# Kernel tuning notes

Hardware: AMD Instinct MI355X
Metric: run time of the kernel (lower is better)

Reference implementation:

```python
import jax, jax.numpy as jnp
import numpy as np

N = 50000      # nodes
E = 800000     # edges (avg degree 16)
D = 64         # input_dim
L = 64         # latent_dim


def setup_inputs() -> dict:
    key = jax.random.key(0)
    k1, k2, k3, k4, k5, k6 = jax.random.split(key, 6)
    x = jax.random.normal(k1, (N, D), dtype=jnp.float32)
    weight = jax.random.normal(k2, (D, L), dtype=jnp.float32) / np.sqrt(D)
    bias = jax.random.normal(k3, (L,), dtype=jnp.float32) * 0.01
    # strictly positive degrees to keep division well-behaved
    node_degree = jax.random.uniform(k4, (N, 1), dtype=jnp.float32) + 1.0
    edge_src = jax.random.randint(k5, (E,), 0, N, dtype=jnp.int32)
    edge_dst = jax.random.randint(k6, (E,), 0, N, dtype=jnp.int32)
    return {"x": x, "weight": weight, "bias": bias,
            "node_degree": node_degree,
            "edge_src": edge_src, "edge_dst": edge_dst}


def reference(x, weight, bias, node_degree, edge_src, edge_dst):
    # gnn_spmm(adj, x): sparse aggregate over incoming edges -> [N, D]
    agg = jax.ops.segment_sum(x[edge_src], edge_dst, num_segments=N)
    pooled = agg + x                      # residual self-connection
    node_linear = pooled @ weight + bias  # dense projection [N, L]
    normalized = node_linear / node_degree  # normalize_embedding == 2
    return jax.nn.relu(normalized)
```

## Files before the change

kernel.cpp:

```cpp
#include <hip/hip_runtime.h>
#include <hip/hip_fp16.h>

#define N_NODES 50000
#define DIM 64
#define CB 391
#define CAP 2560
#define EB 6400
#define PLW 68
#define SCAP 1344

typedef _Float16 half8 __attribute__((ext_vector_type(8)));
typedef _Float16 half4v __attribute__((ext_vector_type(4)));
typedef float floatx4 __attribute__((ext_vector_type(4)));

#define WS_CURSOR  0
#define WS_COARSE  2048
#define WS_XH      (WS_COARSE + 4003840)
#define WS_WT      (WS_XH + 6400000)

__global__ void __launch_bounds__(256) prep_kernel(
        const float* __restrict__ x, const float* __restrict__ W,
        const int* __restrict__ edge_src, const int* __restrict__ edge_dst,
        _Float16* __restrict__ xh, _Float16* __restrict__ wt,
        int* __restrict__ bucket_cursor, unsigned int* __restrict__ coarse,
        int E, int pa) {
    int b = blockIdx.x, t = threadIdx.x;
    if (b < pa) {
        __shared__ int lhist[CB];
        __shared__ int lbase[CB];
        for (int i = t; i < CB; i += 256) lhist[i] = 0;
        __syncthreads();

        int base = b * EB;
        int end = base + EB; if (end > E) end = E;

        for (int i = base + t; i < end; i += 256) {
            atomicAdd(&lhist[edge_dst[i] >> 7], 1);
        }
        __syncthreads();
        for (int i = t; i < CB; i += 256) {
            lbase[i] = atomicAdd(&bucket_cursor[i], lhist[i]);
            lhist[i] = 0;
        }
        __syncthreads();
        for (int i = base + t; i < end; i += 256) {
            int s = edge_src[i];
            int d = edge_dst[i];
            int bk = d >> 7;
            int r = atomicAdd(&lhist[bk], 1);
            coarse[(size_t)bk * CAP + lbase[bk] + r] =
                ((unsigned int)s << 7) | (unsigned int)(d & 127);
        }
    } else if (b < pa + 3125) {
        int i = (b - pa) * 256 + t;
        float4 v = reinterpret_cast<const float4*>(x)[i];
        half4v h = { (_Float16)v.x, (_Float16)v.y, (_Float16)v.z, (_Float16)v.w };
        reinterpret_cast<half4v*>(xh)[i] = h;
    } else {
        #pragma unroll
        for (int i = 0; i < 16; ++i) {
            int idx = t * 16 + i;
            int n = idx >> 6, k = idx & 63;
            wt[idx] = (_Float16)W[k * DIM + n];
        }
    }
}

__global__ void __launch_bounds__(256) fused_kernel(
        const float* __restrict__ x,
        const _Float16* __restrict__ xh,
        const _Float16* __restrict__ wt,
        const float* __restrict__ bias,
        const float* __restrict__ deg,
        const int* __restrict__ bucket_cursor,
        const unsigned int* __restrict__ coarse,
        float* __restrict__ out) {
    __shared__ unsigned int sedges[SCAP];
    __shared__ float pl[64 * PLW];
    __shared__ int hist[64];
    __shared__ int excl[64];
    __shared__ int cur[64];

    int t = threadIdx.x;
    int b = blockIdx.x;
    int bucket = b >> 1;
    int half = b & 1;
    int nb = b * 64;
    int cnt = bucket_cursor[bucket];
    const unsigned int* cbk = coarse + (size_t)bucket * CAP;

    if (t < 64) hist[t] = 0;
    __syncthreads();
    for (int i = t; i < cnt; i += 256) {
        unsigned int e = cbk[i];
        int loc = (int)(e & 127u);
        if ((loc >> 6) == half) atomicAdd(&hist[loc & 63], 1);
    }
    __syncthreads();

    if (t < 64) {
        int v = hist[t];
        int s = v;
        #pragma unroll
        for (int off = 1; off < 64; off <<= 1) {
            int u = __shfl_up(s, off);
            if (t >= off) s += u;
        }
        excl[t] = s - v;
        cur[t]  = s - v;
    }
    __syncthreads();

    for (int i = t; i < cnt; i += 256) {
        unsigned int e = cbk[i];
        int loc = (int)(e & 127u);
        if ((loc >> 6) == half) {
            int p = atomicAdd(&cur[loc & 63], 1);
            sedges[p] = e >> 7;
        }
    }
    __syncthreads();

    int g = t >> 3;
    int c = t & 7;
    #pragma unroll
    for (int pass = 0; pass < 2; ++pass) {
        int loc = g + pass * 32;
        int node = nb + loc;
        float acc[8];
        #pragma unroll
        for (int j = 0; j < 8; ++j) acc[j] = 0.f;
        int off = excl[loc];
        int ct = (node < N_NODES) ? hist[loc] : 0;
        int k = 0;
        for (; k + 4 <= ct; k += 4) {
            int s0 = (int)sedges[off + k + 0];
            int s1 = (int)sedges[off + k + 1];
            int s2 = (int)sedges[off + k + 2];
            int s3 = (int)sedges[off + k + 3];
            half8 v0 = *reinterpret_cast<const half8*>(xh + (size_t)s0 * DIM + c * 8);
            half8 v1 = *reinterpret_cast<const half8*>(xh + (size_t)s1 * DIM + c * 8);
            half8 v2 = *reinterpret_cast<const half8*>(xh + (size_t)s2 * DIM + c * 8);
            half8 v3 = *reinterpret_cast<const half8*>(xh + (size_t)s3 * DIM + c * 8);
            #pragma unroll
            for (int j = 0; j < 8; ++j) {
                acc[j] += (float)v0[j]; acc[j] += (float)v1[j];
                acc[j] += (float)v2[j]; acc[j] += (float)v3[j];
            }
        }
        for (; k < ct; ++k) {
            int s0 = (int)sedges[off + k];
            half8 v0 = *reinterpret_cast<const half8*>(xh + (size_t)s0 * DIM + c * 8);
            #pragma unroll
            for (int j = 0; j < 8; ++j) acc[j] += (float)v0[j];
        }
        if (node < N_NODES) {
            const float4 r0 = *reinterpret_cast<const float4*>(
                x + (size_t)node * DIM + c * 8);
            const float4 r1 = *reinterpret_cast<const float4*>(
                x + (size_t)node * DIM + c * 8 + 4);
            float* p = &pl[loc * PLW + c * 8];
            p[0] = acc[0] + r0.x; p[1] = acc[1] + r0.y;
            p[2] = acc[2] + r0.z; p[3] = acc[3] + r0.w;
            p[4] = acc[4] + r1.x; p[5] = acc[5] + r1.y;
            p[6] = acc[6] + r1.z; p[7] = acc[7] + r1.w;
        }
    }
    __syncthreads();

    int wv = t >> 6;
    int lane = t & 63;
    int m = lane & 15;
    int q = lane >> 4;
    int lbase = wv * 16;

    const float* ap = &pl[(lbase + m) * PLW];
    half8 a0, a1;
    #pragma unroll
    for (int j = 0; j < 8; ++j) a0[j] = (_Float16)ap[q * 8 + j];
    #pragma unroll
    for (int j = 0; j < 8; ++j) a1[j] = (_Float16)ap[32 + q * 8 + j];

    floatx4 acc4[4];
    #pragma unroll
    for (int tt = 0; tt < 4; ++tt) {
        half8 b0 = *reinterpret_cast<const half8*>(wt + (size_t)(tt * 16 + m) * DIM + q * 8);
        half8 b1 = *reinterpret_cast<const half8*>(wt + (size_t)(tt * 16 + m) * DIM + q * 8 + 32);
        floatx4 cfrag = {0.f, 0.f, 0.f, 0.f};
        cfrag = __builtin_amdgcn_mfma_f32_16x16x32_f16(a0, b0, cfrag, 0, 0, 0);
        cfrag = __builtin_amdgcn_mfma_f32_16x16x32_f16(a1, b1, cfrag, 0, 0, 0);
        acc4[tt] = cfrag;
    }

    #pragma unroll
    for (int r = 0; r < 4; ++r) {
        int row = q * 4 + r;
        int node = nb + lbase + row;
        if (node < N_NODES) {
            float inv = 1.0f / deg[node];
            #pragma unroll
            for (int tt = 0; tt < 4; ++tt) {
                float v = (acc4[tt][r] + bias[tt * 16 + m]) * inv;
                out[(size_t)node * DIM + tt * 16 + m] = fmaxf(v, 0.f);
            }
        }
    }
}

extern "C" void kernel_launch(void* const* d_in, const int* in_sizes, int n_in,
                              void* d_out, int out_size, void* d_ws, size_t ws_size,
                              hipStream_t stream) {
    const float* x        = (const float*)d_in[0];
    const float* weight   = (const float*)d_in[1];
    const float* bias     = (const float*)d_in[2];
    const float* node_deg = (const float*)d_in[3];
    const int*   edge_src = (const int*)d_in[4];
    const int*   edge_dst = (const int*)d_in[5];
    float* out = (float*)d_out;
    const int E = in_sizes[4];

    char* ws = (char*)d_ws;
    int*          bucket_cursor = (int*)(ws + WS_CURSOR);
    unsigned int* coarse        = (unsigned int*)(ws + WS_COARSE);
    _Float16*     xh            = (_Float16*)(ws + WS_XH);
    _Float16*     wt            = (_Float16*)(ws + WS_WT);

    hipMemsetAsync(bucket_cursor, 0, CB * sizeof(int), stream);

    int pa = (E + EB - 1) / EB;
    prep_kernel<<<pa + 3125 + 1, 256, 0, stream>>>(
        x, weight, edge_src, edge_dst, xh, wt, bucket_cursor, coarse, E, pa);

    fused_kernel<<<2 * CB, 256, 0, stream>>>(
        x, xh, wt, bias, node_deg, bucket_cursor, coarse, out);
}
```

Measured before the change: 120.1 us.

## Drop fp16 copy of x, gather fp32 directly, split buckets into sub-cursors

Removes the prep pass that converted x to fp16 and gathers the fp32 rows directly in the aggregation, with 16 threads per node over four passes. The edge bucketing now uses smaller edge blocks (1024) and 8 sub-bucket cursors per coarse bucket, so many more prep blocks run with less contention on each global atomic cursor. The fused kernel walks the 8 sub-bucket segments per bucket. This saves the conversion traffic, but each gathered row is twice as many bytes, and the fixed sub-bucket capacity (384) could overflow under skewed degree distributions.

```diff
diff --git a/kernel.cpp b/kernel.cpp
--- a/kernel.cpp
+++ b/kernel.cpp
@@ -4,26 +4,24 @@
 #define N_NODES 50000
 #define DIM 64
 #define CB 391
-#define CAP 2560
-#define EB 6400
+#define SUBS 8
+#define CAPS 384
+#define EB 1024
+#define SCAP 1344
 #define PLW 68
-#define SCAP 1344
 
 typedef _Float16 half8 __attribute__((ext_vector_type(8)));
-typedef _Float16 half4v __attribute__((ext_vector_type(4)));
 typedef float floatx4 __attribute__((ext_vector_type(4)));
 
 #define WS_CURSOR  0
-#define WS_COARSE  2048
-#define WS_XH      (WS_COARSE + 4003840)
-#define WS_WT      (WS_XH + 6400000)
+#define WS_COARSE  16384
+#define WS_WT      (WS_COARSE + 4804608)
 
 __global__ void __launch_bounds__(256) prep_kernel(
-        const float* __restrict__ x, const float* __restrict__ W,
+        const float* __restrict__ W,
         const int* __restrict__ edge_src, const int* __restrict__ edge_dst,
-        _Float16* __restrict__ xh, _Float16* __restrict__ wt,
-        int* __restrict__ bucket_cursor, unsigned int* __restrict__ coarse,
-        int E, int pa) {
+        int* __restrict__ cursor2, unsigned int* __restrict__ coarse2,
+        _Float16* __restrict__ wt, int E, int pa) {
     int b = blockIdx.x, t = threadIdx.x;
     if (b < pa) {
         __shared__ int lhist[CB];
@@ -31,6 +29,7 @@
         for (int i = t; i < CB; i += 256) lhist[i] = 0;
         __syncthreads();
 
+        int sub = b & (SUBS - 1);
         int base = b * EB;
         int end = base + EB; if (end > E) end = E;
 
@@ -39,7 +38,7 @@
         }
         __syncthreads();
         for (int i = t; i < CB; i += 256) {
-            lbase[i] = atomicAdd(&bucket_cursor[i], lhist[i]);
+            lbase[i] = atomicAdd(&cursor2[sub * CB + i], lhist[i]);
             lhist[i] = 0;
         }
         __syncthreads();
@@ -48,14 +47,9 @@
             int d = edge_dst[i];
             int bk = d >> 7;
             int r = atomicAdd(&lhist[bk], 1);
-            coarse[(size_t)bk * CAP + lbase[bk] + r] =
+            coarse2[((size_t)bk * SUBS + sub) * CAPS + lbase[bk] + r] =
                 ((unsigned int)s << 7) | (unsigned int)(d & 127);
         }
-    } else if (b < pa + 3125) {
-        int i = (b - pa) * 256 + t;
-        float4 v = reinterpret_cast<const float4*>(x)[i];
-        half4v h = { (_Float16)v.x, (_Float16)v.y, (_Float16)v.z, (_Float16)v.w };
-        reinterpret_cast<half4v*>(xh)[i] = h;
     } else {
         #pragma unroll
         for (int i = 0; i < 16; ++i) {
@@ -68,12 +62,11 @@
 
 __global__ void __launch_bounds__(256) fused_kernel(
         const float* __restrict__ x,
-        const _Float16* __restrict__ xh,
         const _Float16* __restrict__ wt,
         const float* __restrict__ bias,
         const float* __restrict__ deg,
-        const int* __restrict__ bucket_cursor,
-        const unsigned int* __restrict__ coarse,
+        const int* __restrict__ cursor2,
+        const unsigned int* __restrict__ coarse2,
         float* __restrict__ out) {
     __shared__ unsigned int sedges[SCAP];
     __shared__ float pl[64 * PLW];
@@ -86,15 +79,17 @@
     int bucket = b >> 1;
     int half = b & 1;
     int nb = b * 64;
-    int cnt = bucket_cursor[bucket];
-    const unsigned int* cbk = coarse + (size_t)bucket * CAP;
 
     if (t < 64) hist[t] = 0;
     __syncthreads();
-    for (int i = t; i < cnt; i += 256) {
-        unsigned int e = cbk[i];
-        int loc = (int)(e & 127u);
-        if ((loc >> 6) == half) atomicAdd(&hist[loc & 63], 1);
+    for (int s = 0; s < SUBS; ++s) {
+        int cs = cursor2[s * CB + bucket];
+        const unsigned int* p = coarse2 + ((size_t)bucket * SUBS + s) * CAPS;
+        for (int i = t; i < cs; i += 256) {
+            unsigned int e = p[i];
+            int loc = (int)(e & 127u);
+            if ((loc >> 6) == half) atomicAdd(&hist[loc & 63], 1);
+        }
     }
     __syncthreads();
 
@@ -111,25 +106,27 @@
     }
     __syncthreads();
 
-    for (int i = t; i < cnt; i += 256) {
-        unsigned int e = cbk[i];
-        int loc = (int)(e & 127u);
-        if ((loc >> 6) == half) {
-            int p = atomicAdd(&cur[loc & 63], 1);
-            sedges[p] = e >> 7;
-        }
-    }
-    __syncthreads();
-
-    int g = t >> 3;
-    int c = t & 7;
-    #pragma unroll
-    for (int pass = 0; pass < 2; ++pass) {
-        int loc = g + pass * 32;
+    for (int s = 0; s < SUBS; ++s) {
+        int cs = cursor2[s * CB + bucket];
+        const unsigned int* p = coarse2 + ((size_t)bucket * SUBS + s) * CAPS;
+        for (int i = t; i < cs; i += 256) {
+            unsigned int e = p[i];
+            int loc = (int)(e & 127u);
+            if ((loc >> 6) == half) {
+                int q = atomicAdd(&cur[loc & 63], 1);
+                sedges[q] = e >> 7;
+            }
+        }
+    }
+    __syncthreads();
+
+    int g = t >> 4;
+    int c = t & 15;
+    #pragma unroll
+    for (int pass = 0; pass < 4; ++pass) {
+        int loc = g + pass * 16;
         int node = nb + loc;
-        float acc[8];
-        #pragma unroll
-        for (int j = 0; j < 8; ++j) acc[j] = 0.f;
+        float4 acc = make_float4(0.f, 0.f, 0.f, 0.f);
         int off = excl[loc];
         int ct = (node < N_NODES) ? hist[loc] : 0;
         int k = 0;
@@ -138,32 +135,26 @@
             int s1 = (int)sedges[off + k + 1];
             int s2 = (int)sedges[off + k + 2];
             int s3 = (int)sedges[off + k + 3];
-            half8 v0 = *reinterpret_cast<const half8*>(xh + (size_t)s0 * DIM + c * 8);
-            half8 v1 = *reinterpret_cast<const half8*>(xh + (size_t)s1 * DIM + c * 8);
-            half8 v2 = *reinterpret_cast<const half8*>(xh + (size_t)s2 * DIM + c * 8);
-            half8 v3 = *reinterpret_cast<const half8*>(xh + (size_t)s3 * DIM + c * 8);
-            #pragma unroll
-            for (int j = 0; j < 8; ++j) {
-                acc[j] += (float)v0[j]; acc[j] += (float)v1[j];
-                acc[j] += (float)v2[j]; acc[j] += (float)v3[j];
-            }
+            float4 v0 = *reinterpret_cast<const float4*>(x + (size_t)s0 * DIM + c * 4);
+            float4 v1 = *reinterpret_cast<const float4*>(x + (size_t)s1 * DIM + c * 4);
+            float4 v2 = *reinterpret_cast<const float4*>(x + (size_t)s2 * DIM + c * 4);
+            float4 v3 = *reinterpret_cast<const float4*>(x + (size_t)s3 * DIM + c * 4);
+            acc.x += v0.x + v1.x + v2.x + v3.x;
+            acc.y += v0.y + v1.y + v2.y + v3.y;
+            acc.z += v0.z + v1.z + v2.z + v3.z;
+            acc.w += v0.w + v1.w + v2.w + v3.w;
         }
         for (; k < ct; ++k) {
             int s0 = (int)sedges[off + k];
-            half8 v0 = *reinterpret_cast<const half8*>(xh + (size_t)s0 * DIM + c * 8);
-            #pragma unroll
-            for (int j = 0; j < 8; ++j) acc[j] += (float)v0[j];
+            float4 v0 = *reinterpret_cast<const float4*>(x + (size_t)s0 * DIM + c * 4);
+            acc.x += v0.x; acc.y += v0.y; acc.z += v0.z; acc.w += v0.w;
         }
         if (node < N_NODES) {
-            const float4 r0 = *reinterpret_cast<const float4*>(
-                x + (size_t)node * DIM + c * 8);
-            const float4 r1 = *reinterpret_cast<const float4*>(
-                x + (size_t)node * DIM + c * 8 + 4);
-            float* p = &pl[loc * PLW + c * 8];
-            p[0] = acc[0] + r0.x; p[1] = acc[1] + r0.y;
-            p[2] = acc[2] + r0.z; p[3] = acc[3] + r0.w;
-            p[4] = acc[4] + r1.x; p[5] = acc[5] + r1.y;
-            p[6] = acc[6] + r1.z; p[7] = acc[7] + r1.w;
+            const float4 r = *reinterpret_cast<const float4*>(
+                x + (size_t)node * DIM + c * 4);
+            float* p = &pl[loc * PLW + c * 4];
+            p[0] = acc.x + r.x; p[1] = acc.y + r.y;
+            p[2] = acc.z + r.z; p[3] = acc.w + r.w;
         }
     }
     __syncthreads();
@@ -220,17 +211,16 @@
     const int E = in_sizes[4];
 
     char* ws = (char*)d_ws;
-    int*          bucket_cursor = (int*)(ws + WS_CURSOR);
-    unsigned int* coarse        = (unsigned int*)(ws + WS_COARSE);
-    _Float16*     xh            = (_Float16*)(ws + WS_XH);
-    _Float16*     wt            = (_Float16*)(ws + WS_WT);
-
-    hipMemsetAsync(bucket_cursor, 0, CB * sizeof(int), stream);
+    int*          cursor2 = (int*)(ws + WS_CURSOR);
+    unsigned int* coarse2 = (unsigned int*)(ws + WS_COARSE);
+    _Float16*     wt      = (_Float16*)(ws + WS_WT);
+
+    hipMemsetAsync(cursor2, 0, SUBS * CB * sizeof(int), stream);
 
     int pa = (E + EB - 1) / EB;
-    prep_kernel<<<pa + 3125 + 1, 256, 0, stream>>>(
-        x, weight, edge_src, edge_dst, xh, wt, bucket_cursor, coarse, E, pa);
+    prep_kernel<<<pa + 1, 256, 0, stream>>>(
+        weight, edge_src, edge_dst, cursor2, coarse2, wt, E, pa);
 
     fused_kernel<<<2 * CB, 256, 0, stream>>>(
-        x, xh, wt, bias, node_deg, bucket_cursor, coarse, out);
+        x, wt, bias, node_deg, cursor2, coarse2, out);
 }
```

Result: slower. 125.8 us (+4.7%).

## Coarsen edge buckets to 512 nodes and unroll gather loop by eight

Applied to the files above, without the earlier changes.

Edge binning now uses 98 coarse buckets of 512 destination nodes instead of 391 buckets of 128. This shrinks per-block histogram and cursor atomic work in the prep kernel and gives larger contiguous write regions. Each fused block of 64 nodes must now scan the whole 512-node bucket to filter its edges, adding redundant reads. The neighbor gather loop is also unrolled to 8 outstanding loads to raise memory-level parallelism, at some register cost.

```diff
diff --git a/kernel.cpp b/kernel.cpp
--- a/kernel.cpp
+++ b/kernel.cpp
@@ -3,53 +3,54 @@
 
 #define N_NODES 50000
 #define DIM 64
-#define CB 391
-#define CAP 2560
+#define PB 98
+#define CAP 8960
 #define EB 6400
+#define NB 782
+#define SCAP 1408
 #define PLW 68
-#define SCAP 1344
 
 typedef _Float16 half8 __attribute__((ext_vector_type(8)));
 typedef _Float16 half4v __attribute__((ext_vector_type(4)));
 typedef float floatx4 __attribute__((ext_vector_type(4)));
 
 #define WS_CURSOR  0
-#define WS_COARSE  2048
-#define WS_XH      (WS_COARSE + 4003840)
+#define WS_COARSE  1024
+#define WS_XH      (WS_COARSE + 3512320)
 #define WS_WT      (WS_XH + 6400000)
 
 __global__ void __launch_bounds__(256) prep_kernel(
         const float* __restrict__ x, const float* __restrict__ W,
         const int* __restrict__ edge_src, const int* __restrict__ edge_dst,
+        int* __restrict__ cursor, unsigned int* __restrict__ coarse,
         _Float16* __restrict__ xh, _Float16* __restrict__ wt,
-        int* __restrict__ bucket_cursor, unsigned int* __restrict__ coarse,
         int E, int pa) {
     int b = blockIdx.x, t = threadIdx.x;
     if (b < pa) {
-        __shared__ int lhist[CB];
-        __shared__ int lbase[CB];
-        for (int i = t; i < CB; i += 256) lhist[i] = 0;
+        __shared__ int lhist[PB];
+        __shared__ int lbase[PB];
+        if (t < PB) lhist[t] = 0;
         __syncthreads();
 
         int base = b * EB;
         int end = base + EB; if (end > E) end = E;
 
         for (int i = base + t; i < end; i += 256) {
-            atomicAdd(&lhist[edge_dst[i] >> 7], 1);
+            atomicAdd(&lhist[edge_dst[i] >> 9], 1);
         }
         __syncthreads();
-        for (int i = t; i < CB; i += 256) {
-            lbase[i] = atomicAdd(&bucket_cursor[i], lhist[i]);
-            lhist[i] = 0;
+        if (t < PB) {
+            lbase[t] = atomicAdd(&cursor[t], lhist[t]);
+            lhist[t] = 0;
         }
         __syncthreads();
         for (int i = base + t; i < end; i += 256) {
             int s = edge_src[i];
             int d = edge_dst[i];
-            int bk = d >> 7;
+            int bk = d >> 9;
             int r = atomicAdd(&lhist[bk], 1);
             coarse[(size_t)bk * CAP + lbase[bk] + r] =
-                ((unsigned int)s << 7) | (unsigned int)(d & 127);
+                ((unsigned int)s << 9) | (unsigned int)(d & 511);
         }
     } else if (b < pa + 3125) {
         int i = (b - pa) * 256 + t;
@@ -72,7 +73,7 @@
         const _Float16* __restrict__ wt,
         const float* __restrict__ bias,
         const float* __restrict__ deg,
-        const int* __restrict__ bucket_cursor,
+        const int* __restrict__ cursor,
         const unsigned int* __restrict__ coarse,
         float* __restrict__ out) {
     __shared__ unsigned int sedges[SCAP];
@@ -83,18 +84,18 @@
 
     int t = threadIdx.x;
     int b = blockIdx.x;
-    int bucket = b >> 1;
-    int half = b & 1;
+    int pb = b >> 3;
+    int sub = b & 7;
     int nb = b * 64;
-    int cnt = bucket_cursor[bucket];
-    const unsigned int* cbk = coarse + (size_t)bucket * CAP;
+    int cnt = cursor[pb];
+    const unsigned int* cbk = coarse + (size_t)pb * CAP;
 
     if (t < 64) hist[t] = 0;
     __syncthreads();
     for (int i = t; i < cnt; i += 256) {
         unsigned int e = cbk[i];
-        int loc = (int)(e & 127u);
-        if ((loc >> 6) == half) atomicAdd(&hist[loc & 63], 1);
+        int loc = (int)(e & 511u);
+        if ((loc >> 6) == sub) atomicAdd(&hist[loc & 63], 1);
     }
     __syncthreads();
 
@@ -113,10 +114,10 @@
 
     for (int i = t; i < cnt; i += 256) {
         unsigned int e = cbk[i];
-        int loc = (int)(e & 127u);
-        if ((loc >> 6) == half) {
+        int loc = (int)(e & 511u);
+        if ((loc >> 6) == sub) {
             int p = atomicAdd(&cur[loc & 63], 1);
-            sedges[p] = e >> 7;
+            sedges[p] = e >> 9;
         }
     }
     __syncthreads();
@@ -133,20 +134,18 @@
         int off = excl[loc];
         int ct = (node < N_NODES) ? hist[loc] : 0;
         int k = 0;
-        for (; k + 4 <= ct; k += 4) {
-            int s0 = (int)sedges[off + k + 0];
-            int s1 = (int)sedges[off + k + 1];
-            int s2 = (int)sedges[off + k + 2];
-            int s3 = (int)sedges[off + k + 3];
-            half8 v0 = *reinterpret_cast<const half8*>(xh + (size_t)s0 * DIM + c * 8);
-            half8 v1 = *reinterpret_cast<const half8*>(xh + (size_t)s1 * DIM + c * 8);
-            half8 v2 = *reinterpret_cast<const half8*>(xh + (size_t)s2 * DIM + c * 8);
-            half8 v3 = *reinterpret_cast<const half8*>(xh + (size_t)s3 * DIM + c * 8);
-            #pragma unroll
-            for (int j = 0; j < 8; ++j) {
-                acc[j] += (float)v0[j]; acc[j] += (float)v1[j];
-                acc[j] += (float)v2[j]; acc[j] += (float)v3[j];
-            }
+        for (; k + 8 <= ct; k += 8) {
+            int sid[8];
+            #pragma unroll
+            for (int u = 0; u < 8; ++u) sid[u] = (int)sedges[off + k + u];
+            half8 v[8];
+            #pragma unroll
+            for (int u = 0; u < 8; ++u)
+                v[u] = *reinterpret_cast<const half8*>(xh + (size_t)sid[u] * DIM + c * 8);
+            #pragma unroll
+            for (int u = 0; u < 8; ++u)
+                #pragma unroll
+                for (int j = 0; j < 8; ++j) acc[j] += (float)v[u][j];
         }
         for (; k < ct; ++k) {
             int s0 = (int)sedges[off + k];
@@ -220,17 +219,17 @@
     const int E = in_sizes[4];
 
     char* ws = (char*)d_ws;
-    int*          bucket_cursor = (int*)(ws + WS_CURSOR);
-    unsigned int* coarse        = (unsigned int*)(ws + WS_COARSE);
-    _Float16*     xh            = (_Float16*)(ws + WS_XH);
-    _Float16*     wt            = (_Float16*)(ws + WS_WT);
-
-    hipMemsetAsync(bucket_cursor, 0, CB * sizeof(int), stream);
+    int*          cursor = (int*)(ws + WS_CURSOR);
+    unsigned int* coarse = (unsigned int*)(ws + WS_COARSE);
+    _Float16*     xh     = (_Float16*)(ws + WS_XH);
+    _Float16*     wt     = (_Float16*)(ws + WS_WT);
+
+    hipMemsetAsync(cursor, 0, PB * sizeof(int), stream);
 
     int pa = (E + EB - 1) / EB;
     prep_kernel<<<pa + 3125 + 1, 256, 0, stream>>>(
-        x, weight, edge_src, edge_dst, xh, wt, bucket_cursor, coarse, E, pa);
-
-    fused_kernel<<<2 * CB, 256, 0, stream>>>(
-        x, xh, wt, bias, node_deg, bucket_cursor, coarse, out);
+        x, weight, edge_src, edge_dst, cursor, coarse, xh, wt, E, pa);
+
+    fused_kernel<<<NB, 256, 0, stream>>>(
+        x, xh, wt, bias, node_deg, cursor, coarse, out);
 }
```

After: 135.0 us. 12.4% more time.
